# Optimization experiments

Measured on AMD Instinct MI355X. Metric: run time of the kernel, lower is better.

The kernel has to match this reference:

```python
import jax, jax.numpy as jnp
import numpy as np

N_NODES = 10000
N_EDGES = 100000
D_IN = 2 * 1280   # concat of row/col node embeddings
H1 = 512
H2 = 256


def gcn_conv(x, edge_index, W, b):
    """PyG GCNConv: add self-loops, symmetric deg^-1/2 normalization,
    x @ W then scatter-add of normalized messages, plus bias.
    num_nodes is inferred from x.shape[0] (here = n_edges, faithful to source)."""
    N = x.shape[0]
    loops = jnp.arange(N, dtype=edge_index.dtype)
    row = jnp.concatenate([edge_index[0], loops])  # sources
    col = jnp.concatenate([edge_index[1], loops])  # targets
    deg = jax.ops.segment_sum(jnp.ones_like(row, dtype=x.dtype), col, num_segments=N)
    dinv = jax.lax.rsqrt(deg)  # deg >= 1 thanks to self-loops
    norm = dinv[row] * dinv[col]  # [E+N]
    h = x @ W  # [N, out]
    out = jax.ops.segment_sum(h[row] * norm[:, None], col, num_segments=N)
    return out + b


def setup_inputs() -> dict:
    key = jax.random.key(0)
    ks = jax.random.split(key, 9)
    x = jax.random.normal(ks[0], (N_NODES, 1280), dtype=jnp.float32)
    edge_index = jax.random.randint(ks[1], (2, N_EDGES), 0, N_NODES, dtype=jnp.int32)
    # uniform noise for gumbel-sigmoid (torch.rand); keep strictly in (0,1)
    eps = jax.random.uniform(ks[2], (N_EDGES, 1), jnp.float32, 1e-6, 1.0 - 1e-6)
    W1 = jax.random.normal(ks[3], (D_IN, H1), jnp.float32) * (1.0 / np.sqrt(D_IN))
    b1 = jnp.zeros((H1,), jnp.float32)
    W2 = jax.random.normal(ks[4], (H1, H2), jnp.float32) * (1.0 / np.sqrt(H1))
    b2 = jnp.zeros((H2,), jnp.float32)
    Wl = jax.random.normal(ks[5], (H2, 1), jnp.float32) * (1.0 / np.sqrt(H2))
    bl = jnp.zeros((1,), jnp.float32)
    return {"x": x, "edge_index": edge_index, "eps": eps,
            "W1": W1, "b1": b1, "W2": W2, "b2": b2, "Wl": Wl, "bl": bl}


def reference(x, edge_index, eps, W1, b1, W2, b2, Wl, bl):
    rows, cols = edge_index[0], edge_index[1]
    # per-edge explainer input: concat of endpoint embeddings -> [E, 2560]
    input_embs = jnp.concatenate([x[rows], x[cols]], axis=1)
    h = jax.nn.relu(gcn_conv(input_embs, edge_index, W1, b1))
    h = jax.nn.relu(gcn_conv(h, edge_index, W2, b2))
    pre = h @ Wl + bl  # [E, 1] sampling weights
    # gumbel-sigmoid sampling (temperature = 1.0)
    gate = jnp.log(eps) - jnp.log1p(-eps) + pre
    mask = jax.nn.sigmoid(gate)
    pos, neg = mask, 1.0 - mask
    kld = jnp.mean(pos * jnp.log(pos / 0.5 + 1e-8) + neg * jnp.log(neg / 0.5 + 1e-9))
    return (kld, mask)
```

## Files before the change

### kernel.cpp

```cpp
#include <hip/hip_runtime.h>
#include <cstdint>
#include <cstddef>

#define H1DIM 512
#define H2DIM 256
#define DNODE 1280
#define NPACK 1024

typedef __attribute__((ext_vector_type(8))) short short8v;
typedef __attribute__((ext_vector_type(4))) float f32x4;
typedef __attribute__((ext_vector_type(4))) unsigned short us4;

__device__ __forceinline__ unsigned short f2bf(float f) {
    unsigned int u = __builtin_bit_cast(unsigned int, f);
    u += 0x7fffu + ((u >> 16) & 1u);
    return (unsigned short)(u >> 16);
}
__device__ __forceinline__ float bf2f(unsigned short h) {
    unsigned int u = ((unsigned int)h) << 16;
    return __builtin_bit_cast(float, u);
}

__device__ __forceinline__ int cmi(int R, int kq) {
    return ((R >> 4) << 9) + (((kq >> 3) << 4) + (R & 15)) * 8;
}

__global__ void hist_k(const int* __restrict__ e1, int* __restrict__ hist, int E) {
    int e = blockIdx.x * 256 + threadIdx.x;
    if (e < E) atomicAdd(&hist[e1[e]], 1);
}
__global__ __launch_bounds__(1024) void scan_dinv_k(
    const int* __restrict__ hist, int* __restrict__ off, int* __restrict__ cursor,
    float* __restrict__ dinv, int N)
{
    __shared__ int part[1024];
    const int t = threadIdx.x;
    const int per = (N + 1023) / 1024;
    const int base = t * per;
    int s = 0;
    for (int i = 0; i < per; ++i) { int b = base + i; if (b < N) s += hist[b]; }
    part[t] = s;
    __syncthreads();
    for (int d = 1; d < 1024; d <<= 1) {
        int v = (t >= d) ? part[t - d] : 0;
        __syncthreads();
        part[t] += v;
        __syncthreads();
    }
    int run = (t == 0) ? 0 : part[t - 1];
    for (int i = 0; i < per; ++i) {
        int b = base + i;
        if (b < N) {
            int h = hist[b];
            off[b] = run;
            run += h;
            cursor[b] = 0;
            dinv[b] = rsqrtf(1.0f + (float)h);
        }
    }
    if (t == 1023) off[N] = run;
}
__global__ void fill_k(const int* __restrict__ e0, const int* __restrict__ e1,
                       const int* __restrict__ off, int* __restrict__ cursor,
                       int* __restrict__ srcs, int E) {
    int e = blockIdx.x * 256 + threadIdx.x;
    if (e < E) {
        int t = e1[e];
        int p = off[t] + atomicAdd(&cursor[t], 1);
        srcs[p] = e0[e];
    }
}

__global__ void cvt_x_k(const float* __restrict__ src, unsigned short* __restrict__ dst, int n) {
    int i = blockIdx.x * 256 + threadIdx.x;
    if (i * 4 < n) {
        f32x4 v = *reinterpret_cast<const f32x4*>(src + (size_t)i * 4);
        us4 o;
        o[0] = f2bf(v.x); o[1] = f2bf(v.y); o[2] = f2bf(v.z); o[3] = f2bf(v.w);
        *reinterpret_cast<us4*>(dst + (size_t)i * 4) = o;
    }
}

__global__ __launch_bounds__(256) void transpose_cvt_k(
    const float* __restrict__ src, unsigned short* __restrict__ dst, int ldsrc, int lddst)
{
    __shared__ float tile[32][33];
    const int c0 = blockIdx.x * 32;
    const int r0 = blockIdx.y * 32;
    const int tx = threadIdx.x & 31;
    const int ty = threadIdx.x >> 5;
#pragma unroll
    for (int rr = ty; rr < 32; rr += 8)
        tile[rr][tx] = src[(size_t)(r0 + rr) * ldsrc + c0 + tx];
    __syncthreads();
#pragma unroll
    for (int rr = ty; rr < 32; rr += 8)
        dst[(size_t)(c0 + rr) * lddst + r0 + tx] = f2bf(tile[tx][rr]);
}

template <int MODE>
__global__ __launch_bounds__(512) void gemm_u_k(
    const unsigned short* __restrict__ Ab,
    const unsigned short* __restrict__ Bt,
    unsigned short* __restrict__ Cb,
    const unsigned short* __restrict__ out1b,
    const unsigned short* __restrict__ XWb16,
    const float* __restrict__ b1,
    const float* __restrict__ b2,
    const float* __restrict__ Wl,
    const int* __restrict__ e0, const int* __restrict__ e1,
    unsigned short* __restrict__ h2b, float* __restrict__ pre_raw,
    int M, int K, int Nn, int nwg)
{
    __shared__ alignas(16) unsigned short As[2][128 * 32];
    __shared__ alignas(16) unsigned short Bs[2][256 * 32];
    __shared__ float b1s[H1DIM];
    __shared__ float b2s[H2DIM];
    __shared__ float wls[H2DIM];
    __shared__ float preacc[128];

    const int tid  = threadIdx.x;
    const int lane = tid & 63;
    const int w    = tid >> 6;
    const int wm   = w >> 2, wn = w & 3;

    int mb, n0;
    if (MODE == 0) {
        const int q = nwg >> 3, r = nwg & 7;
        const int xcd = blockIdx.x & 7;
        const int base = (xcd < r) ? xcd * (q + 1) : r * (q + 1) + (xcd - r) * q;
        const int wg = base + (blockIdx.x >> 3);
        mb = wg >> 2;
        n0 = (wg & 3) << 8;
    } else {
        mb = blockIdx.x;
        n0 = 0;
    }
    const int m0 = mb * 128;

    if (MODE == 1) {
        if (tid < 128) preacc[tid] = 0.f;
        if (tid < 256) { b2s[tid] = b2[tid]; wls[tid] = Wl[tid]; }
        b1s[tid] = b1[tid];
    }

    const int sa_r = tid >> 2, sa_k = (tid & 3) << 3;
    const int sb_r = tid >> 1, sb_k = (tid & 1) << 4;
    const int gma  = m0 + sa_r;
    const bool aval = (gma < M);

    const int aw  = cmi(sa_r, sa_k);
    const int bw0 = cmi(sb_r, sb_k);
    const int bw1 = cmi(sb_r, sb_k + 8);

    const unsigned short* bsrc = Bt + (size_t)(n0 + sb_r) * K + sb_k;
    const unsigned short* s1 = nullptr;
    const unsigned short* s2 = nullptr;
    bool dual = false;
    if (MODE == 0) {
        if (aval) s1 = Ab + (size_t)gma * K + sa_k;
    } else if (aval) {
        if (gma < Nn) {
            s1 = out1b + (size_t)gma * H1DIM + sa_k;
        } else {
            s1 = XWb16 + (size_t)e0[gma] * NPACK + sa_k;
            s2 = XWb16 + (size_t)e1[gma] * NPACK + H1DIM + sa_k;
            dual = true;
        }
    }
    if (MODE == 1) __syncthreads();

    f32x4 acc[4][4];
#pragma unroll
    for (int i = 0; i < 4; ++i)
#pragma unroll
        for (int j = 0; j < 4; ++j) acc[i][j] = f32x4{0.f, 0.f, 0.f, 0.f};

    short8v ab1, ab2, bb0, bb1;

    auto load_tile = [&](int k0) {
        bb0 = *reinterpret_cast<const short8v*>(bsrc + k0);
        bb1 = *reinterpret_cast<const short8v*>(bsrc + k0 + 8);
        if (aval) {
            ab1 = *reinterpret_cast<const short8v*>(s1 + k0);
            if (MODE == 1 && dual) ab2 = *reinterpret_cast<const short8v*>(s2 + k0);
        }
    };
    auto write_lds = [&](int buf, int k0) {
        *reinterpret_cast<short8v*>(&Bs[buf][bw0]) = bb0;
        *reinterpret_cast<short8v*>(&Bs[buf][bw1]) = bb1;
        short8v av;
        if (!aval) {
            av = short8v{0,0,0,0,0,0,0,0};
        } else if (MODE == 0 || !dual) {
            av = ab1;
        } else {
#pragma unroll
            for (int ii = 0; ii < 8; ++ii) {
                float v = bf2f((unsigned short)ab1[ii]) + bf2f((unsigned short)ab2[ii])
                        + b1s[k0 + sa_k + ii];
                v = fmaxf(v, 0.f);
                av[ii] = (short)f2bf(v);
            }
        }
        *reinterpret_cast<short8v*>(&As[buf][aw]) = av;
    };

    load_tile(0);
    int buf = 0;
    for (int k0 = 0; k0 < K; k0 += 32) {
        write_lds(buf, k0);
        __syncthreads();
        if (k0 + 32 < K) load_tile(k0 + 32);

        const unsigned short* ard = &As[buf][(wm * 4) * 512 + lane * 8];
        const unsigned short* brd = &Bs[buf][(wn * 4) * 512 + lane * 8];
        short8v af[4], bfq[4];
#pragma unroll
        for (int i = 0; i < 4; ++i)
            af[i] = *reinterpret_cast<const short8v*>(ard + i * 512);
#pragma unroll
        for (int j = 0; j < 4; ++j)
            bfq[j] = *reinterpret_cast<const short8v*>(brd + j * 512);
#pragma unroll
        for (int i = 0; i < 4; ++i)
#pragma unroll
            for (int j = 0; j < 4; ++j)
                acc[i][j] = __builtin_amdgcn_mfma_f32_16x16x32_bf16(af[i], bfq[j], acc[i][j], 0, 0, 0);
        buf ^= 1;
    }

    const int crow0 = m0 + wm * 64 + ((lane >> 4) << 2);
    if (MODE == 0) {
        const int ccol = n0 + wn * 64 + (lane & 15);
#pragma unroll
        for (int i = 0; i < 4; ++i)
#pragma unroll
            for (int q = 0; q < 4; ++q) {
                const int row = crow0 + i * 16 + q;
                if (row < M) {
#pragma unroll
                    for (int j = 0; j < 4; ++j)
                        Cb[(size_t)row * NPACK + ccol + j * 16] = f2bf(acc[i][j][q]);
                }
            }
    } else {
        const int cbase = wn * 64 + (lane & 15);
#pragma unroll
        for (int i = 0; i < 4; ++i)
#pragma unroll
            for (int q = 0; q < 4; ++q) {
                float v = 0.f;
#pragma unroll
                for (int j = 0; j < 4; ++j) {
                    const int c = cbase + j * 16;
                    v += fmaxf(acc[i][j][q] + b2s[c], 0.f) * wls[c];
                }
                v += __shfl_xor(v, 1, 64);
                v += __shfl_xor(v, 2, 64);
                v += __shfl_xor(v, 4, 64);
                v += __shfl_xor(v, 8, 64);
                if ((lane & 15) == 0)
                    atomicAdd(&preacc[wm * 64 + i * 16 + ((lane >> 4) << 2) + q], v);
            }
        if (m0 < Nn) {
            const int ccol = wn * 64 + (lane & 15);
#pragma unroll
            for (int i = 0; i < 4; ++i)
#pragma unroll
                for (int q = 0; q < 4; ++q) {
                    const int row = crow0 + i * 16 + q;
                    if (row < Nn) {
#pragma unroll
                        for (int j = 0; j < 4; ++j)
                            h2b[(size_t)row * H2DIM + ccol + j * 16] = f2bf(acc[i][j][q]);
                    }
                }
        }
        __syncthreads();
        if (tid < 128) {
            const int gm = m0 + tid;
            if (gm >= Nn && gm < M) pre_raw[gm] = preacc[tid];
        }
    }
}

__global__ __launch_bounds__(256) void build1_k(
    const unsigned short* __restrict__ XWb16, const float* __restrict__ dinv,
    const int* __restrict__ e0, const int* __restrict__ e1,
    unsigned short* __restrict__ H1b)
{
    const int r = blockIdx.x;
    const int a = e0[r], b = e1[r];
    const float dv = dinv[r];
    const unsigned short* pt = XWb16 + (size_t)a * NPACK;
    const unsigned short* pb = XWb16 + (size_t)b * NPACK + H1DIM;
    const int j = threadIdx.x * 2;
    const unsigned ut = *reinterpret_cast<const unsigned*>(pt + j);
    const unsigned ub = *reinterpret_cast<const unsigned*>(pb + j);
    const float ox = (bf2f((unsigned short)(ut & 0xffff)) + bf2f((unsigned short)(ub & 0xffff))) * dv;
    const float oy = (bf2f((unsigned short)(ut >> 16))   + bf2f((unsigned short)(ub >> 16)))   * dv;
    const unsigned pk = (unsigned)f2bf(ox) | ((unsigned)f2bf(oy) << 16);
    *reinterpret_cast<unsigned*>(H1b + (size_t)r * H1DIM + j) = pk;
}

__global__ __launch_bounds__(256) void agg1_k(
    const unsigned short* __restrict__ H1b, const int* __restrict__ off, const int* __restrict__ srcs,
    const float* __restrict__ b1, const float* __restrict__ dinv,
    unsigned short* __restrict__ out1b)
{
    const int t = blockIdx.x;
    const int j = threadIdx.x * 2;
    const int s0 = off[t], s1e = off[t + 1];
    const float dt = dinv[t];
    const unsigned u0 = *reinterpret_cast<const unsigned*>(H1b + (size_t)t * H1DIM + j);
    float ax = bf2f((unsigned short)(u0 & 0xffff));
    float ay = bf2f((unsigned short)(u0 >> 16));
    for (int i = s0; i < s1e; ++i) {
        const unsigned v = *reinterpret_cast<const unsigned*>(H1b + (size_t)srcs[i] * H1DIM + j);
        ax += bf2f((unsigned short)(v & 0xffff));
        ay += bf2f((unsigned short)(v >> 16));
    }
    const float ox = fmaxf(b1[j]     + dt * ax, 0.f);
    const float oy = fmaxf(b1[j + 1] + dt * ay, 0.f);
    const unsigned pk = (unsigned)f2bf(ox) | ((unsigned)f2bf(oy) << 16);
    *reinterpret_cast<unsigned*>(out1b + (size_t)t * H1DIM + j) = pk;
}

__global__ __launch_bounds__(128) void agg2_k(
    const unsigned short* __restrict__ h2b, const int* __restrict__ off, const int* __restrict__ srcs,
    const float* __restrict__ b2, const float* __restrict__ Wl,
    const float* __restrict__ dinv, float* __restrict__ pre_low)
{
    __shared__ float part[2];
    const int t = blockIdx.x;
    const int j = threadIdx.x * 2;
    const int s0 = off[t], s1e = off[t + 1];
    const float dt = dinv[t];
    const unsigned u0 = *reinterpret_cast<const unsigned*>(h2b + (size_t)t * H2DIM + j);
    float ax = bf2f((unsigned short)(u0 & 0xffff)) * dt;
    float ay = bf2f((unsigned short)(u0 >> 16)) * dt;
    for (int i = s0; i < s1e; ++i) {
        const int s = srcs[i];
        const float ds = dinv[s];
        const unsigned v = *reinterpret_cast<const unsigned*>(h2b + (size_t)s * H2DIM + j);
        ax += bf2f((unsigned short)(v & 0xffff)) * ds;
        ay += bf2f((unsigned short)(v >> 16)) * ds;
    }
    float p = fmaxf(b2[j]     + dt * ax, 0.f) * Wl[j]
            + fmaxf(b2[j + 1] + dt * ay, 0.f) * Wl[j + 1];
#pragma unroll
    for (int o = 32; o; o >>= 1) p += __shfl_down(p, o, 64);
    if ((threadIdx.x & 63) == 0) part[threadIdx.x >> 6] = p;
    __syncthreads();
    if (threadIdx.x == 0) pre_low[t] = part[0] + part[1];
}

__global__ __launch_bounds__(256) void final2_k(
    const float* __restrict__ pre_low, const float* __restrict__ pre_raw,
    const float* __restrict__ blp, const float* __restrict__ eps,
    float* __restrict__ dout, int E, int Nn)
{
    __shared__ float part[4];
    const int i = blockIdx.x * 256 + threadIdx.x;
    float kld = 0.f;
    if (i < E) {
        const float pre = ((i < Nn) ? pre_low[i] : pre_raw[i]) + blp[0];
        const float ee = eps[i];
        const float gate = logf(ee) - log1pf(-ee) + pre;
        const float m = 1.0f / (1.0f + expf(-gate));
        dout[1 + i] = m;
        const float pos = m, neg = 1.0f - m;
        kld = pos * logf(pos * 2.0f + 1e-8f) + neg * logf(neg * 2.0f + 1e-9f);
    }
#pragma unroll
    for (int o = 32; o; o >>= 1) kld += __shfl_down(kld, o, 64);
    const int lane = threadIdx.x & 63, wv = threadIdx.x >> 6;
    if (lane == 0) part[wv] = kld;
    __syncthreads();
    if (threadIdx.x == 0)
        atomicAdd(&dout[0], (part[0] + part[1] + part[2] + part[3]) / (float)E);
}

extern "C" void kernel_launch(void* const* d_in, const int* in_sizes, int n_in,
                              void* d_out, int out_size, void* d_ws, size_t ws_size,
                              hipStream_t stream)
{
    const float* x   = (const float*)d_in[0];
    const int*   ei  = (const int*)d_in[1];
    const float* eps = (const float*)d_in[2];
    const float* W1  = (const float*)d_in[3];
    const float* b1  = (const float*)d_in[4];
    const float* W2  = (const float*)d_in[5];
    const float* b2  = (const float*)d_in[6];
    const float* Wl  = (const float*)d_in[7];
    const float* bl  = (const float*)d_in[8];
    float* out = (float*)d_out;
    float* ws  = (float*)d_ws;

    const int N = in_sizes[0] / DNODE;
    const int E = in_sizes[1] / 2;
    const int* e0 = ei;
    const int* e1 = ei + E;

    float* dinv     = ws;
    float* pre_raw  = dinv + 16384;
    float* pre_low  = pre_raw + E;
    float* fend     = pre_low + 16384;
    unsigned short* XWb16 = (unsigned short*)fend;
    unsigned short* out1b = XWb16 + (size_t)N * NPACK;
    unsigned short* H1b   = out1b + (size_t)N * H1DIM;
    unsigned short* h2b   = H1b + (size_t)N * H1DIM;
    unsigned short* xb    = h2b + (size_t)N * H2DIM;
    unsigned short* Bpt1  = xb + (size_t)N * DNODE;
    unsigned short* W2t   = Bpt1 + (size_t)NPACK * DNODE;
    int* hist   = (int*)(W2t + (size_t)H2DIM * H1DIM);
    int* cursor = hist + N;
    int* off    = cursor + N;
    int* srcs   = off + (N + 1);

    hipMemsetAsync(hist, 0, (size_t)N * sizeof(int), stream);
    hipMemsetAsync(out, 0, sizeof(float), stream);

    hist_k<<<(E + 255) / 256, 256, 0, stream>>>(e1, hist, E);
    scan_dinv_k<<<1, 1024, 0, stream>>>(hist, off, cursor, dinv, N);
    fill_k<<<(E + 255) / 256, 256, 0, stream>>>(e0, e1, off, cursor, srcs, E);

    cvt_x_k<<<(N * DNODE / 4 + 255) / 256, 256, 0, stream>>>(x, xb, N * DNODE);
    transpose_cvt_k<<<dim3(H1DIM / 32, DNODE / 32), 256, 0, stream>>>(W1, Bpt1, H1DIM, DNODE);
    transpose_cvt_k<<<dim3(H1DIM / 32, DNODE / 32), 256, 0, stream>>>(
        W1 + (size_t)DNODE * H1DIM, Bpt1 + (size_t)H1DIM * DNODE, H1DIM, DNODE);
    transpose_cvt_k<<<dim3(H2DIM / 32, H1DIM / 32), 256, 0, stream>>>(W2, W2t, H2DIM, H1DIM);

    {
        const int nwg = 4 * ((N + 127) / 128);
        gemm_u_k<0><<<nwg, 512, 0, stream>>>(
            xb, Bpt1, XWb16, nullptr, nullptr, b1, b2, Wl, e0, e1,
            nullptr, nullptr, N, DNODE, 0, nwg);
    }

    build1_k<<<N, 256, 0, stream>>>(XWb16, dinv, e0, e1, H1b);
    agg1_k<<<N, 256, 0, stream>>>(H1b, off, srcs, b1, dinv, out1b);

    {
        const int nwg = (E + 127) / 128;
        gemm_u_k<1><<<nwg, 512, 0, stream>>>(
            nullptr, W2t, nullptr, out1b, XWb16, b1, b2, Wl, e0, e1,
            h2b, pre_raw, E, H1DIM, N, nwg);
    }

    agg2_k<<<N, 128, 0, stream>>>(h2b, off, srcs, b2, Wl, dinv, pre_low);

    final2_k<<<(E + 255) / 256, 256, 0, stream>>>(pre_low, pre_raw, bl, eps, out, E, N);
}
```

Before: 218.9 us.

## Merge prep kernels into one launch and fuse edge-build into aggregation

Folds the x bf16 conversion, degree histogram and three weight transpose-convert kernels into a single launch that dispatches on block index. It also removes the build1 kernel and its intermediate H1 buffer. The first-layer aggregation now recomputes each source row's message directly from the packed XW product using two gathers and a dinv scale. This cuts launch overhead and one full write and read of the intermediate, at the cost of twice the gathers per neighbour in the aggregation loop.

```diff
diff --git a/kernel.cpp b/kernel.cpp
--- a/kernel.cpp
+++ b/kernel.cpp
@@ -25,10 +25,6 @@
     return ((R >> 4) << 9) + (((kq >> 3) << 4) + (R & 15)) * 8;
 }
 
-__global__ void hist_k(const int* __restrict__ e1, int* __restrict__ hist, int E) {
-    int e = blockIdx.x * 256 + threadIdx.x;
-    if (e < E) atomicAdd(&hist[e1[e]], 1);
-}
 __global__ __launch_bounds__(1024) void scan_dinv_k(
     const int* __restrict__ hist, int* __restrict__ off, int* __restrict__ cursor,
     float* __restrict__ dinv, int N)
@@ -71,22 +67,45 @@
     }
 }
 
-__global__ void cvt_x_k(const float* __restrict__ src, unsigned short* __restrict__ dst, int n) {
-    int i = blockIdx.x * 256 + threadIdx.x;
-    if (i * 4 < n) {
-        f32x4 v = *reinterpret_cast<const f32x4*>(src + (size_t)i * 4);
-        us4 o;
-        o[0] = f2bf(v.x); o[1] = f2bf(v.y); o[2] = f2bf(v.z); o[3] = f2bf(v.w);
-        *reinterpret_cast<us4*>(dst + (size_t)i * 4) = o;
-    }
-}
-
-__global__ __launch_bounds__(256) void transpose_cvt_k(
-    const float* __restrict__ src, unsigned short* __restrict__ dst, int ldsrc, int lddst)
+__global__ __launch_bounds__(256) void prep_k(
+    const float* __restrict__ x, unsigned short* __restrict__ xb, int ncvt, int ntot,
+    const int* __restrict__ e1, int* __restrict__ hist, int nhist, int E,
+    const float* __restrict__ W1, unsigned short* __restrict__ Bpt1,
+    const float* __restrict__ W2, unsigned short* __restrict__ W2t)
 {
     __shared__ float tile[32][33];
-    const int c0 = blockIdx.x * 32;
-    const int r0 = blockIdx.y * 32;
+    int b = blockIdx.x;
+
+    if (b < ncvt) {
+        int i = b * 256 + threadIdx.x;
+        if (i * 4 < ntot) {
+            f32x4 v = *reinterpret_cast<const f32x4*>(x + (size_t)i * 4);
+            us4 o;
+            o[0] = f2bf(v.x); o[1] = f2bf(v.y); o[2] = f2bf(v.z); o[3] = f2bf(v.w);
+            *reinterpret_cast<us4*>(xb + (size_t)i * 4) = o;
+        }
+        return;
+    }
+    b -= ncvt;
+    if (b < nhist) {
+        int e = b * 256 + threadIdx.x;
+        if (e < E) atomicAdd(&hist[e1[e]], 1);
+        return;
+    }
+    b -= nhist;
+
+    const float* src; unsigned short* dst; int ldsrc, lddst, bx, by;
+    if (b < 640) {
+        src = W1; dst = Bpt1; ldsrc = H1DIM; lddst = DNODE; bx = b & 15; by = b >> 4;
+    } else if (b < 1280) {
+        b -= 640;
+        src = W1 + (size_t)DNODE * H1DIM; dst = Bpt1 + (size_t)H1DIM * DNODE;
+        ldsrc = H1DIM; lddst = DNODE; bx = b & 15; by = b >> 4;
+    } else {
+        b -= 1280;
+        src = W2; dst = W2t; ldsrc = H2DIM; lddst = H1DIM; bx = b & 7; by = b >> 3;
+    }
+    const int c0 = bx * 32, r0 = by * 32;
     const int tx = threadIdx.x & 31;
     const int ty = threadIdx.x >> 5;
 #pragma unroll
@@ -285,27 +304,9 @@
     }
 }
 
-__global__ __launch_bounds__(256) void build1_k(
-    const unsigned short* __restrict__ XWb16, const float* __restrict__ dinv,
+__global__ __launch_bounds__(256) void agg1_k(
+    const unsigned short* __restrict__ XWb16, const int* __restrict__ off, const int* __restrict__ srcs,
     const int* __restrict__ e0, const int* __restrict__ e1,
-    unsigned short* __restrict__ H1b)
-{
-    const int r = blockIdx.x;
-    const int a = e0[r], b = e1[r];
-    const float dv = dinv[r];
-    const unsigned short* pt = XWb16 + (size_t)a * NPACK;
-    const unsigned short* pb = XWb16 + (size_t)b * NPACK + H1DIM;
-    const int j = threadIdx.x * 2;
-    const unsigned ut = *reinterpret_cast<const unsigned*>(pt + j);
-    const unsigned ub = *reinterpret_cast<const unsigned*>(pb + j);
-    const float ox = (bf2f((unsigned short)(ut & 0xffff)) + bf2f((unsigned short)(ub & 0xffff))) * dv;
-    const float oy = (bf2f((unsigned short)(ut >> 16))   + bf2f((unsigned short)(ub >> 16)))   * dv;
-    const unsigned pk = (unsigned)f2bf(ox) | ((unsigned)f2bf(oy) << 16);
-    *reinterpret_cast<unsigned*>(H1b + (size_t)r * H1DIM + j) = pk;
-}
-
-__global__ __launch_bounds__(256) void agg1_k(
-    const unsigned short* __restrict__ H1b, const int* __restrict__ off, const int* __restrict__ srcs,
     const float* __restrict__ b1, const float* __restrict__ dinv,
     unsigned short* __restrict__ out1b)
 {
@@ -313,13 +314,20 @@
     const int j = threadIdx.x * 2;
     const int s0 = off[t], s1e = off[t + 1];
     const float dt = dinv[t];
-    const unsigned u0 = *reinterpret_cast<const unsigned*>(H1b + (size_t)t * H1DIM + j);
-    float ax = bf2f((unsigned short)(u0 & 0xffff));
-    float ay = bf2f((unsigned short)(u0 >> 16));
+    float ax, ay;
+    {
+        const unsigned ut = *reinterpret_cast<const unsigned*>(XWb16 + (size_t)e0[t] * NPACK + j);
+        const unsigned ub = *reinterpret_cast<const unsigned*>(XWb16 + (size_t)e1[t] * NPACK + H1DIM + j);
+        ax = (bf2f((unsigned short)(ut & 0xffff)) + bf2f((unsigned short)(ub & 0xffff))) * dt;
+        ay = (bf2f((unsigned short)(ut >> 16))   + bf2f((unsigned short)(ub >> 16)))   * dt;
+    }
     for (int i = s0; i < s1e; ++i) {
-        const unsigned v = *reinterpret_cast<const unsigned*>(H1b + (size_t)srcs[i] * H1DIM + j);
-        ax += bf2f((unsigned short)(v & 0xffff));
-        ay += bf2f((unsigned short)(v >> 16));
+        const int s = srcs[i];
+        const float ds = dinv[s];
+        const unsigned ut = *reinterpret_cast<const unsigned*>(XWb16 + (size_t)e0[s] * NPACK + j);
+        const unsigned ub = *reinterpret_cast<const unsigned*>(XWb16 + (size_t)e1[s] * NPACK + H1DIM + j);
+        ax += (bf2f((unsigned short)(ut & 0xffff)) + bf2f((unsigned short)(ub & 0xffff))) * ds;
+        ay += (bf2f((unsigned short)(ut >> 16))   + bf2f((unsigned short)(ub >> 16)))   * ds;
     }
     const float ox = fmaxf(b1[j]     + dt * ax, 0.f);
     const float oy = fmaxf(b1[j + 1] + dt * ay, 0.f);
@@ -409,8 +417,7 @@
     float* fend     = pre_low + 16384;
     unsigned short* XWb16 = (unsigned short*)fend;
     unsigned short* out1b = XWb16 + (size_t)N * NPACK;
-    unsigned short* H1b   = out1b + (size_t)N * H1DIM;
-    unsigned short* h2b   = H1b + (size_t)N * H1DIM;
+    unsigned short* h2b   = out1b + (size_t)N * H1DIM;
     unsigned short* xb    = h2b + (size_t)N * H2DIM;
     unsigned short* Bpt1  = xb + (size_t)N * DNODE;
     unsigned short* W2t   = Bpt1 + (size_t)NPACK * DNODE;
@@ -422,15 +429,17 @@
     hipMemsetAsync(hist, 0, (size_t)N * sizeof(int), stream);
     hipMemsetAsync(out, 0, sizeof(float), stream);
 
-    hist_k<<<(E + 255) / 256, 256, 0, stream>>>(e1, hist, E);
+    {
+        const int ntot = N * DNODE;
+        const int ncvt = (ntot / 4 + 255) / 256;
+        const int nhist = (E + 255) / 256;
+        const int ntr = 640 + 640 + 128;
+        prep_k<<<ncvt + nhist + ntr, 256, 0, stream>>>(
+            x, xb, ncvt, ntot, e1, hist, nhist, E, W1, Bpt1, W2, W2t);
+    }
+
     scan_dinv_k<<<1, 1024, 0, stream>>>(hist, off, cursor, dinv, N);
     fill_k<<<(E + 255) / 256, 256, 0, stream>>>(e0, e1, off, cursor, srcs, E);
-
-    cvt_x_k<<<(N * DNODE / 4 + 255) / 256, 256, 0, stream>>>(x, xb, N * DNODE);
-    transpose_cvt_k<<<dim3(H1DIM / 32, DNODE / 32), 256, 0, stream>>>(W1, Bpt1, H1DIM, DNODE);
-    transpose_cvt_k<<<dim3(H1DIM / 32, DNODE / 32), 256, 0, stream>>>(
-        W1 + (size_t)DNODE * H1DIM, Bpt1 + (size_t)H1DIM * DNODE, H1DIM, DNODE);
-    transpose_cvt_k<<<dim3(H2DIM / 32, H1DIM / 32), 256, 0, stream>>>(W2, W2t, H2DIM, H1DIM);
 
     {
         const int nwg = 4 * ((N + 127) / 128);
@@ -439,8 +448,7 @@
             nullptr, nullptr, N, DNODE, 0, nwg);
     }
 
-    build1_k<<<N, 256, 0, stream>>>(XWb16, dinv, e0, e1, H1b);
-    agg1_k<<<N, 256, 0, stream>>>(H1b, off, srcs, b1, dinv, out1b);
+    agg1_k<<<N, 256, 0, stream>>>(XWb16, off, srcs, e0, e1, b1, dinv, out1b);
 
     {
         const int nwg = (E + 127) / 128;
```

Result: no change. 217.3 us (-0.7%).
